# Optimization experiments

Measured on AMD Instinct MI355X. Metric: run time of the kernel, lower is better.

The kernel has to match this reference:

```python
import jax, jax.numpy as jnp
import numpy as np

D_MODEL = 768
N_HEADS = 12
D_HEAD = D_MODEL // N_HEADS

def setup_inputs() -> dict:
    key = jax.random.key(0)
    ks = jax.random.split(key, 5)
    B, T = 2, 4096
    x = jax.random.normal(ks[0], (B, T, D_MODEL), dtype=jnp.float32)
    s_in = 1.0 / np.sqrt(D_MODEL)
    W_qkv = jax.random.normal(ks[1], (D_MODEL, 3 * D_MODEL), dtype=jnp.float32) * s_in
    b_qkv = jnp.zeros((3 * D_MODEL,), dtype=jnp.float32)
    W_proj = jax.random.normal(ks[2], (D_MODEL, D_MODEL), dtype=jnp.float32) * s_in
    b_proj = jnp.zeros((D_MODEL,), dtype=jnp.float32)
    return {"x": x, "W_qkv": W_qkv, "b_qkv": b_qkv, "W_proj": W_proj, "b_proj": b_proj}

def reference(x, W_qkv, b_qkv, W_proj, b_proj):
    B, T, C = x.shape
    qkv = x @ W_qkv + b_qkv                      # [B,T,3C]
    q, k, v = jnp.split(qkv, 3, axis=-1)
    def heads(t):
        return t.reshape(B, T, N_HEADS, D_HEAD).transpose(0, 2, 1, 3)  # [B,H,T,d]
    q, k, v = heads(q), heads(k), heads(v)
    scale = 1.0 / np.sqrt(D_HEAD)
    att = jnp.einsum('bhqd,bhkd->bhqk', q, k) * scale  # [B,H,T,T]
    causal = jnp.tril(jnp.ones((T, T), dtype=bool))
    att = jnp.where(causal[None, None], att, -jnp.inf)
    att = jax.nn.softmax(att, axis=-1)
    y = jnp.einsum('bhqk,bhkd->bhqd', att, v)          # [B,H,T,d]
    y = y.transpose(0, 2, 1, 3).reshape(B, T, C)
    return y @ W_proj + b_proj
```

## Files before the change

kernel.cpp:

```cpp
#include <hip/hip_runtime.h>
#include <hip/hip_bf16.h>

typedef __bf16 bf16_t;
typedef bf16_t bf16x4 __attribute__((ext_vector_type(4)));
typedef bf16_t bf16x8 __attribute__((ext_vector_type(8)));
typedef float  f32x4  __attribute__((ext_vector_type(4)));

#define TSEQ   4096
#define NBATCH 2
#define DMODEL 768
#define NHEADS 12
#define DHEAD  64
#define NTOK   (NBATCH*TSEQ)
#define NQKV   (3*DMODEL)

#define QSCALE 0.18033688011112042f
#define SMAX 24.0f

__device__ __forceinline__ f32x4 mfma16(bf16x8 a, bf16x8 b, f32x4 c) {
  return __builtin_amdgcn_mfma_f32_16x16x32_bf16(a, b, c, 0, 0, 0);
}

__device__ __forceinline__ void glds16(const bf16_t* g, bf16_t* l) {
  __builtin_amdgcn_global_load_lds(
      (const __attribute__((address_space(1))) void*)g,
      (__attribute__((address_space(3))) void*)l, 16, 0, 0);
}

__global__ __launch_bounds__(256) void k_prep(
    const float* __restrict__ W1, bf16_t* __restrict__ O1,
    const float* __restrict__ W2, bf16_t* __restrict__ O2,
    const float* __restrict__ X, bf16_t* __restrict__ Xb) {
  __shared__ bf16_t tile[64][66];
  int t = blockIdx.x;
  if (t >= 576) {
    const int idx = (t - 576) * 256 + threadIdx.x;
#pragma unroll
    for (int it = 0; it < 2; ++it) {
      const long c = (long)idx + (long)it * 393216;
      const float4 v0 = *(const float4*)(X + c * 8);
      const float4 v1 = *(const float4*)(X + c * 8 + 4);
      bf16x8 o;
      o[0] = (bf16_t)v0.x; o[1] = (bf16_t)v0.y;
      o[2] = (bf16_t)v0.z; o[3] = (bf16_t)v0.w;
      o[4] = (bf16_t)v1.x; o[5] = (bf16_t)v1.y;
      o[6] = (bf16_t)v1.z; o[7] = (bf16_t)v1.w;
      *(bf16x8*)(Xb + c * 8) = o;
    }
    return;
  }
  const float* in; bf16_t* out; int R, C, c0, r0;
  if (t < 432) { in = W1; out = O1; R = DMODEL; C = NQKV;
                 c0 = (t % 36) * 64; r0 = (t / 36) * 64; }
  else { t -= 432; in = W2; out = O2; R = DMODEL; C = DMODEL;
         c0 = (t % 12) * 64; r0 = (t / 12) * 64; }
  const int tid = threadIdx.x;
  const int r = tid >> 2, cb = (tid & 3) * 16;
  const float* ip = in + (long)(r0 + r) * C + c0 + cb;
#pragma unroll
  for (int k = 0; k < 16; k += 4) {
    float4 v = *(const float4*)(ip + k);
    tile[r][cb + k + 0] = (bf16_t)v.x;
    tile[r][cb + k + 1] = (bf16_t)v.y;
    tile[r][cb + k + 2] = (bf16_t)v.z;
    tile[r][cb + k + 3] = (bf16_t)v.w;
  }
  __syncthreads();
  const int c = tid >> 2, rb = (tid & 3) * 16;
  bf16_t* op = out + (long)(c0 + c) * R + r0 + rb;
  bf16x8 v0, v1;
#pragma unroll
  for (int i = 0; i < 8; ++i) { v0[i] = tile[rb + i][c]; v1[i] = tile[rb + 8 + i][c]; }
  *(bf16x8*)(op) = v0;
  *(bf16x8*)(op + 8) = v1;
}

__global__ __launch_bounds__(256) void k_gemm_qkv(
    const bf16_t* __restrict__ Xb, const bf16_t* __restrict__ Bt,
    const float* __restrict__ bias,
    bf16_t* __restrict__ Qo, bf16_t* __restrict__ Ko, bf16_t* __restrict__ Vt) {
  __shared__ __align__(16) bf16_t As[2 * 128 * 32];
  __shared__ __align__(16) bf16_t Bs[2 * 128 * 32];
  const int wave = threadIdx.x >> 6;
  const int lane = threadIdx.x & 63;
  const int quad = lane >> 4;
  const int l16  = lane & 15;
  const int m0 = blockIdx.x * 128;
  const int n0 = blockIdx.y * 128;

  const int srow4  = lane >> 2;
  const int schunk = (lane & 3) ^ ((lane >> 3) & 3);
  const bf16_t* a0 = Xb + (long)(m0 + wave * 32 + srow4) * DMODEL + schunk * 8;
  const bf16_t* b0 = Bt + (long)(n0 + wave * 32 + srow4) * DMODEL + schunk * 8;

  f32x4 acc[2][8] = {};

  glds16(a0,               As + (wave * 32) * 32);
  glds16(a0 + 16 * DMODEL, As + (wave * 32 + 16) * 32);
  glds16(b0,               Bs + (wave * 32) * 32);
  glds16(b0 + 16 * DMODEL, Bs + (wave * 32 + 16) * 32);
  __syncthreads();

  const int sw = (l16 >> 1) & 3;
  for (int ks = 0; ks < DMODEL / 32; ++ks) {
    const int p = ks & 1;
    if (ks + 1 < DMODEL / 32) {
      const int k1 = (ks + 1) * 32;
      bf16_t* Asx = (p ? As : As + 128 * 32);
      bf16_t* Bsx = (p ? Bs : Bs + 128 * 32);
      glds16(a0 + k1,               Asx + (wave * 32) * 32);
      glds16(a0 + 16 * DMODEL + k1, Asx + (wave * 32 + 16) * 32);
      glds16(b0 + k1,               Bsx + (wave * 32) * 32);
      glds16(b0 + 16 * DMODEL + k1, Bsx + (wave * 32 + 16) * 32);
    }
    const bf16_t* Ap = As + p * (128 * 32);
    const bf16_t* Bp = Bs + p * (128 * 32);

    bf16x8 af0 = *(const bf16x8*)(Ap + (wave * 32 + l16) * 32 + ((quad ^ sw) << 3));
    bf16x8 af1 = *(const bf16x8*)(Ap + (wave * 32 + 16 + l16) * 32 + ((quad ^ sw) << 3));
#pragma unroll
    for (int nt = 0; nt < 8; ++nt) {
      bf16x8 bfm = *(const bf16x8*)(Bp + (nt * 16 + l16) * 32 + ((quad ^ sw) << 3));
      acc[0][nt] = mfma16(af0, bfm, acc[0][nt]);
      acc[1][nt] = mfma16(af1, bfm, acc[1][nt]);
    }
    __syncthreads();
  }

#pragma unroll
  for (int s = 0; s < 2; ++s)
#pragma unroll
    for (int nt = 0; nt < 8; ++nt) {
      const int n = n0 + nt * 16 + l16;
      const float bv = bias[n];
      const int mb = m0 + wave * 32 + s * 16 + quad * 4;
      const int b = mb >> 12;
      const int t = mb & 4095;
      if (n < DMODEL) {
        const int h = n >> 6, d = n & 63;
        bf16_t* qp = Qo + (((long)(b * NHEADS + h) * TSEQ + t) << 6) + d;
#pragma unroll
        for (int j = 0; j < 4; ++j)
          qp[(long)j << 6] = (bf16_t)((acc[s][nt][j] + bv) * QSCALE);
      } else if (n < 2 * DMODEL) {
        const int n2 = n - DMODEL, h = n2 >> 6, d = n2 & 63;
        bf16_t* kp = Ko + (((long)(b * NHEADS + h) * TSEQ + t) << 6) + d;
#pragma unroll
        for (int j = 0; j < 4; ++j)
          kp[(long)j << 6] = (bf16_t)(acc[s][nt][j] + bv);
      } else {
        const int n2 = n - 2 * DMODEL, h = n2 >> 6, d = n2 & 63;
        bf16x4 v;
#pragma unroll
        for (int j = 0; j < 4; ++j) v[j] = (bf16_t)(acc[s][nt][j] + bv);
        *(bf16x4*)(Vt + ((long)(b * NHEADS + h) * DHEAD + d) * TSEQ + t) = v;
      }
    }
}

__global__ __launch_bounds__(256) void k_gemm_proj(
    const bf16_t* __restrict__ P0, const bf16_t* __restrict__ P1,
    const float* __restrict__ L0, const float* __restrict__ L1,
    const bf16_t* __restrict__ Bt, const float* __restrict__ bias,
    float* __restrict__ out) {
  __shared__ __align__(16) bf16_t A0s[2 * 64 * 32];
  __shared__ __align__(16) bf16_t A1s[2 * 64 * 32];
  __shared__ __align__(16) bf16_t Bs[2 * 128 * 32];
  __shared__ float linv[NHEADS * 64];
  const int wave = threadIdx.x >> 6;
  const int lane = threadIdx.x & 63;
  const int quad = lane >> 4;
  const int l16  = lane & 15;
  const int m0 = blockIdx.x * 64;
  const int n0 = blockIdx.y * 128;
  const int b  = m0 >> 12;
  const int t0 = m0 & 4095;

  for (int i = threadIdx.x; i < NHEADS * 64; i += 256) {
    const int h = i >> 6, t = i & 63;
    const long idx = (long)(b * NHEADS + h) * TSEQ + t0 + t;
    linv[i] = 1.f / (L0[idx] + L1[idx]);
  }

  const int srow = lane >> 2;
  const int scol = (lane & 3) * 8;
  const bf16_t* b0 = Bt + (long)(n0 + wave * 16 + srow) * DMODEL + scol;
  const long arowbase = (long)(t0 + wave * 16 + srow);

  f32x4 acc[8] = {};

  {
    const long off = (((long)(b * NHEADS + 0) * TSEQ + arowbase) << 6) + scol;
    glds16(P0 + off, A0s + wave * 16 * 32);
    glds16(P1 + off, A1s + wave * 16 * 32);
  }
  glds16(b0,               Bs + wave * 16 * 32);
  glds16(b0 + 64 * DMODEL, Bs + (64 + wave * 16) * 32);
  __syncthreads();

  for (int ks = 0; ks < DMODEL / 32; ++ks) {
    const int p = ks & 1;
    if (ks + 1 < DMODEL / 32) {
      const int k1 = (ks + 1) * 32;
      const int ksn = ks + 1;
      bf16_t* A0x = (p ? A0s : A0s + 64 * 32);
      bf16_t* A1x = (p ? A1s : A1s + 64 * 32);
      bf16_t* Bsx = (p ? Bs : Bs + 128 * 32);
      const long off = (((long)(b * NHEADS + (ksn >> 1)) * TSEQ + arowbase) << 6)
                       + ((ksn & 1) << 5) + scol;
      glds16(P0 + off, A0x + wave * 16 * 32);
      glds16(P1 + off, A1x + wave * 16 * 32);
      glds16(b0 + k1,               Bsx + wave * 16 * 32);
      glds16(b0 + 64 * DMODEL + k1, Bsx + (64 + wave * 16) * 32);
    }
    const bf16_t* A0p = A0s + p * (64 * 32);
    const bf16_t* A1p = A1s + p * (64 * 32);
    const bf16_t* Bp  = Bs + p * (128 * 32);

    bf16x8 a0 = *(const bf16x8*)(A0p + (wave * 16 + l16) * 32 + quad * 8);
    bf16x8 a1 = *(const bf16x8*)(A1p + (wave * 16 + l16) * 32 + quad * 8);
    const float li = linv[(ks >> 1) * 64 + wave * 16 + l16];
    bf16x8 af;
#pragma unroll
    for (int j = 0; j < 8; ++j)
      af[j] = (bf16_t)(((float)a0[j] + (float)a1[j]) * li);
#pragma unroll
    for (int nt = 0; nt < 8; ++nt) {
      bf16x8 bfm = *(const bf16x8*)(Bp + (nt * 16 + l16) * 32 + quad * 8);
      acc[nt] = mfma16(af, bfm, acc[nt]);
    }
    __syncthreads();
  }

#pragma unroll
  for (int nt = 0; nt < 8; ++nt) {
    const int n = n0 + nt * 16 + l16;
    const float bv = bias[n];
#pragma unroll
    for (int j = 0; j < 4; ++j) {
      const int m = m0 + wave * 16 + quad * 4 + j;
      out[(long)m * DMODEL + n] = acc[nt][j] + bv;
    }
  }
}

__global__ __launch_bounds__(256, 4) void k_attn(
    const bf16_t* __restrict__ Q, const bf16_t* __restrict__ K,
    const bf16_t* __restrict__ Vt,
    bf16_t* __restrict__ P0, bf16_t* __restrict__ P1,
    float* __restrict__ L0, float* __restrict__ L1) {
  __shared__ __align__(16) bf16_t kbuf[2][64 * 64];
  __shared__ __align__(16) bf16_t vbuf[2][64 * 64];
  const int wave = threadIdx.x >> 6;
  const int lane = threadIdx.x & 63;
  const int quad = lane >> 4;
  const int l16  = lane & 15;
  const int bh = blockIdx.x;
  const int qt = 31 - (blockIdx.y >> 1);
  const int sp = blockIdx.y & 1;
  const int niter = qt + 1;
  const int c0 = sp * niter;
  bf16_t* Pp = sp ? P1 : P0;
  float*  Lp = sp ? L1 : L0;

  const bf16_t* Qh = Q + ((long)bh * TSEQ << 6);
  const bf16_t* Kh = K + ((long)bh * TSEQ << 6);
  const bf16_t* Vh = Vt + (long)bh * DHEAD * TSEQ;

  const int qbase = qt * 128 + wave * 32;

  bf16x8 qf[2][2];
#pragma unroll
  for (int s = 0; s < 2; ++s) {
    const bf16_t* qrow = Qh + ((long)(qbase + s * 16 + l16) << 6);
    qf[s][0] = *(const bf16x8*)(qrow + quad * 8);
    qf[s][1] = *(const bf16x8*)(qrow + 32 + quad * 8);
  }

  f32x4 acc[2][4] = {};
  float lS[2] = {0.f, 0.f};
  const f32x4 minit = {-SMAX, -SMAX, -SMAX, -SMAX};

  const int kperm = ((l16 >> 2) << 3) + (l16 & 3);
  const int swl = l16 & 7;
  const int srow = lane >> 3;
  const int cV = (lane & 7) ^ (srow & 7);
  const int cK0 = (lane & 7) ^ (srow & 3);
  const int cK1 = cK0 ^ 4;
  const int r0a = wave * 16, r0b = wave * 16 + 8;

  {
    const int k00 = c0 << 6;
    glds16(Kh + ((long)(k00 + r0a + srow) << 6) + cK0 * 8, &kbuf[0][r0a * 64]);
    glds16(Kh + ((long)(k00 + r0b + srow) << 6) + cK1 * 8, &kbuf[0][r0b * 64]);
    glds16(Vh + (long)(r0a + srow) * TSEQ + k00 + cV * 8,  &vbuf[0][r0a * 64]);
    glds16(Vh + (long)(r0b + srow) * TSEQ + k00 + cV * 8,  &vbuf[0][r0b * 64]);
  }
  __syncthreads();

  for (int ci = 0; ci < niter; ++ci) {
    const int p = ci & 1;
    const int k0 = (c0 + ci) << 6;
    if (ci + 1 < niter) {
      const int k1 = k0 + 64;
      glds16(Kh + ((long)(k1 + r0a + srow) << 6) + cK0 * 8, &kbuf[1 - p][r0a * 64]);
      glds16(Kh + ((long)(k1 + r0b + srow) << 6) + cK1 * 8, &kbuf[1 - p][r0b * 64]);
      glds16(Vh + (long)(r0a + srow) * TSEQ + k1 + cV * 8,  &vbuf[1 - p][r0a * 64]);
      glds16(Vh + (long)(r0b + srow) * TSEQ + k1 + cV * 8,  &vbuf[1 - p][r0b * 64]);
    }
    const bf16_t* kb = kbuf[p];
    const bf16_t* vb = vbuf[p];

#pragma unroll
    for (int g = 0; g < 2; ++g) {
      const int rw0 = (g * 32 + kperm) * 64;
      const int rw1 = (g * 32 + 4 + kperm) * 64;
      bf16x8 kf00 = *(const bf16x8*)(kb + rw0 + ((quad ^ swl) << 3));
      bf16x8 kf01 = *(const bf16x8*)(kb + rw0 + (((quad + 4) ^ swl) << 3));
      bf16x8 kf10 = *(const bf16x8*)(kb + rw1 + ((quad ^ swl) << 3));
      bf16x8 kf11 = *(const bf16x8*)(kb + rw1 + (((quad + 4) ^ swl) << 3));
      const bool domask = (k0 + g * 32 + 31 > qbase);

      bf16x8 pf[2];
#pragma unroll
      for (int s = 0; s < 2; ++s) {
        f32x4 st0 = minit, st1 = minit;
        st0 = mfma16(kf00, qf[s][0], st0);
        st0 = mfma16(kf01, qf[s][1], st0);
        st1 = mfma16(kf10, qf[s][0], st1);
        st1 = mfma16(kf11, qf[s][1], st1);
        if (domask) {
          const int qS = qbase + s * 16 + l16;
          const int kb0 = k0 + g * 32 + quad * 8;
#pragma unroll
          for (int j = 0; j < 4; ++j) {
            if (kb0 + j > qS)     st0[j] = -1e30f;
            if (kb0 + 4 + j > qS) st1[j] = -1e30f;
          }
        }
        float rs = 0.f;
#pragma unroll
        for (int j = 0; j < 4; ++j) {
          float e0 = __builtin_amdgcn_exp2f(st0[j]);
          float e1 = __builtin_amdgcn_exp2f(st1[j]);
          rs += e0 + e1;
          pf[s][j]     = (bf16_t)e0;
          pf[s][4 + j] = (bf16_t)e1;
        }
        lS[s] += rs;
      }
#pragma unroll
      for (int dt = 0; dt < 4; ++dt) {
        const int row = dt * 16 + l16;
        bf16x8 vf = *(const bf16x8*)(vb + row * 64 + ((((g << 2) + quad) ^ swl) << 3));
#pragma unroll
        for (int s = 0; s < 2; ++s)
          acc[s][dt] = mfma16(vf, pf[s], acc[s][dt]);
      }
    }
    __syncthreads();
  }

#pragma unroll
  for (int s = 0; s < 2; ++s) {
    lS[s] += __shfl_xor(lS[s], 16);
    lS[s] += __shfl_xor(lS[s], 32);
  }
#pragma unroll
  for (int s = 0; s < 2; ++s) {
    const int qS = qbase + s * 16 + l16;
    bf16_t* prow = Pp + (((long)bh * TSEQ + qS) << 6);
#pragma unroll
    for (int dt = 0; dt < 4; ++dt) {
      bf16x4 w;
#pragma unroll
      for (int j = 0; j < 4; ++j) w[j] = (bf16_t)acc[s][dt][j];
      *(bf16x4*)(prow + dt * 16 + quad * 4) = w;
    }
    if (quad == 0) Lp[(long)bh * TSEQ + qS] = lS[s];
  }
}

extern "C" void kernel_launch(void* const* d_in, const int* in_sizes, int n_in,
                              void* d_out, int out_size, void* d_ws, size_t ws_size,
                              hipStream_t stream) {
  (void)in_sizes; (void)n_in; (void)out_size; (void)ws_size;
  const float* x     = (const float*)d_in[0];
  const float* Wqkv  = (const float*)d_in[1];
  const float* bqkv  = (const float*)d_in[2];
  const float* Wproj = (const float*)d_in[3];
  const float* bproj = (const float*)d_in[4];
  float* out = (float*)d_out;

  char* ws = (char*)d_ws;
  bf16_t* wqkv_t  = (bf16_t*)ws; ws += (long)NQKV * DMODEL * 2;
  bf16_t* wproj_t = (bf16_t*)ws; ws += (long)DMODEL * DMODEL * 2;
  bf16_t* Xb      = (bf16_t*)ws; ws += (long)NTOK * DMODEL * 2;
  bf16_t* Qb      = (bf16_t*)ws; ws += (long)NTOK * DMODEL * 2;
  bf16_t* Kb      = (bf16_t*)ws; ws += (long)NTOK * DMODEL * 2;
  bf16_t* Vtb     = (bf16_t*)ws; ws += (long)NTOK * DMODEL * 2;
  bf16_t* P0b     = (bf16_t*)ws; ws += (long)NTOK * DMODEL * 2;
  bf16_t* P1b     = (bf16_t*)ws; ws += (long)NTOK * DMODEL * 2;
  float*  L0b     = (float*)ws;  ws += (long)NHEADS * NBATCH * TSEQ * 4;
  float*  L1b     = (float*)ws;  ws += (long)NHEADS * NBATCH * TSEQ * 4;

  k_prep<<<576 + 1536, 256, 0, stream>>>(Wqkv, wqkv_t, Wproj, wproj_t, x, Xb);
  k_gemm_qkv<<<dim3(NTOK / 128, NQKV / 128), 256, 0, stream>>>(Xb, wqkv_t, bqkv, Qb, Kb, Vtb);
  k_attn<<<dim3(NBATCH * NHEADS, 64), 256, 0, stream>>>(Qb, Kb, Vtb, P0b, P1b, L0b, L1b);
  k_gemm_proj<<<dim3(NTOK / 64, DMODEL / 128), 256, 0, stream>>>(
      P0b, P1b, L0b, L1b, wproj_t, bproj, out);
}
```

Before: 218.0 us.

## Split split-K combine into separate kernel and enlarge proj GEMM tile with LDS swizzle

Moves the merge of the two attention partial outputs and the normalisation by the summed softmax denominators out of the projection GEMM into a standalone k_combine kernel. That kernel writes a token-major bf16 activation buffer. The projection GEMM then reads one A operand instead of two, uses 128x128 tiles with two M sub-tiles per wave, and applies an XOR swizzle on LDS chunks to reduce bank conflicts. This adds an extra kernel launch and a full write and read of the combined activation through memory, in exchange for fewer A loads and more MFMA work per B fragment in the GEMM.

```diff
diff --git a/kernel.cpp b/kernel.cpp
--- a/kernel.cpp
+++ b/kernel.cpp
@@ -158,90 +158,88 @@
     }
 }
 
-__global__ __launch_bounds__(256) void k_gemm_proj(
+__global__ __launch_bounds__(256) void k_combine(
     const bf16_t* __restrict__ P0, const bf16_t* __restrict__ P1,
     const float* __restrict__ L0, const float* __restrict__ L1,
-    const bf16_t* __restrict__ Bt, const float* __restrict__ bias,
-    float* __restrict__ out) {
-  __shared__ __align__(16) bf16_t A0s[2 * 64 * 32];
-  __shared__ __align__(16) bf16_t A1s[2 * 64 * 32];
+    bf16_t* __restrict__ Ab) {
+  const int bh = blockIdx.x;
+  const int t  = blockIdx.y * 32 + (threadIdx.x >> 3);
+  const int d0 = (threadIdx.x & 7) * 8;
+  const long lidx = (long)bh * TSEQ + t;
+  const float li = 1.f / (L0[lidx] + L1[lidx]);
+  const long pidx = (lidx << 6) + d0;
+  bf16x8 a = *(const bf16x8*)(P0 + pidx);
+  bf16x8 b = *(const bf16x8*)(P1 + pidx);
+  bf16x8 o;
+#pragma unroll
+  for (int j = 0; j < 8; ++j)
+    o[j] = (bf16_t)(((float)a[j] + (float)b[j]) * li);
+  const int bb = bh / NHEADS, h = bh % NHEADS;
+  *(bf16x8*)(Ab + (long)(bb * TSEQ + t) * DMODEL + h * 64 + d0) = o;
+}
+
+__global__ __launch_bounds__(256) void k_gemm_proj(
+    const bf16_t* __restrict__ Ab, const bf16_t* __restrict__ Bt,
+    const float* __restrict__ bias, float* __restrict__ out) {
+  __shared__ __align__(16) bf16_t As[2 * 128 * 32];
   __shared__ __align__(16) bf16_t Bs[2 * 128 * 32];
-  __shared__ float linv[NHEADS * 64];
   const int wave = threadIdx.x >> 6;
   const int lane = threadIdx.x & 63;
   const int quad = lane >> 4;
   const int l16  = lane & 15;
-  const int m0 = blockIdx.x * 64;
+  const int m0 = blockIdx.x * 128;
   const int n0 = blockIdx.y * 128;
-  const int b  = m0 >> 12;
-  const int t0 = m0 & 4095;
-
-  for (int i = threadIdx.x; i < NHEADS * 64; i += 256) {
-    const int h = i >> 6, t = i & 63;
-    const long idx = (long)(b * NHEADS + h) * TSEQ + t0 + t;
-    linv[i] = 1.f / (L0[idx] + L1[idx]);
-  }
-
-  const int srow = lane >> 2;
-  const int scol = (lane & 3) * 8;
-  const bf16_t* b0 = Bt + (long)(n0 + wave * 16 + srow) * DMODEL + scol;
-  const long arowbase = (long)(t0 + wave * 16 + srow);
-
-  f32x4 acc[8] = {};
-
-  {
-    const long off = (((long)(b * NHEADS + 0) * TSEQ + arowbase) << 6) + scol;
-    glds16(P0 + off, A0s + wave * 16 * 32);
-    glds16(P1 + off, A1s + wave * 16 * 32);
-  }
-  glds16(b0,               Bs + wave * 16 * 32);
-  glds16(b0 + 64 * DMODEL, Bs + (64 + wave * 16) * 32);
+
+  const int srow4  = lane >> 2;
+  const int schunk = (lane & 3) ^ ((lane >> 3) & 3);
+  const bf16_t* a0 = Ab + (long)(m0 + wave * 32 + srow4) * DMODEL + schunk * 8;
+  const bf16_t* b0 = Bt + (long)(n0 + wave * 32 + srow4) * DMODEL + schunk * 8;
+
+  f32x4 acc[2][8] = {};
+
+  glds16(a0,               As + (wave * 32) * 32);
+  glds16(a0 + 16 * DMODEL, As + (wave * 32 + 16) * 32);
+  glds16(b0,               Bs + (wave * 32) * 32);
+  glds16(b0 + 16 * DMODEL, Bs + (wave * 32 + 16) * 32);
   __syncthreads();
 
+  const int sw = (l16 >> 1) & 3;
   for (int ks = 0; ks < DMODEL / 32; ++ks) {
     const int p = ks & 1;
     if (ks + 1 < DMODEL / 32) {
       const int k1 = (ks + 1) * 32;
-      const int ksn = ks + 1;
-      bf16_t* A0x = (p ? A0s : A0s + 64 * 32);
-      bf16_t* A1x = (p ? A1s : A1s + 64 * 32);
+      bf16_t* Asx = (p ? As : As + 128 * 32);
       bf16_t* Bsx = (p ? Bs : Bs + 128 * 32);
-      const long off = (((long)(b * NHEADS + (ksn >> 1)) * TSEQ + arowbase) << 6)
-                       + ((ksn & 1) << 5) + scol;
-      glds16(P0 + off, A0x + wave * 16 * 32);
-      glds16(P1 + off, A1x + wave * 16 * 32);
-      glds16(b0 + k1,               Bsx + wave * 16 * 32);
-      glds16(b0 + 64 * DMODEL + k1, Bsx + (64 + wave * 16) * 32);
-    }
-    const bf16_t* A0p = A0s + p * (64 * 32);
-    const bf16_t* A1p = A1s + p * (64 * 32);
-    const bf16_t* Bp  = Bs + p * (128 * 32);
-
-    bf16x8 a0 = *(const bf16x8*)(A0p + (wave * 16 + l16) * 32 + quad * 8);
-    bf16x8 a1 = *(const bf16x8*)(A1p + (wave * 16 + l16) * 32 + quad * 8);
-    const float li = linv[(ks >> 1) * 64 + wave * 16 + l16];
-    bf16x8 af;
-#pragma unroll
-    for (int j = 0; j < 8; ++j)
-      af[j] = (bf16_t)(((float)a0[j] + (float)a1[j]) * li);
+      glds16(a0 + k1,               Asx + (wave * 32) * 32);
+      glds16(a0 + 16 * DMODEL + k1, Asx + (wave * 32 + 16) * 32);
+      glds16(b0 + k1,               Bsx + (wave * 32) * 32);
+      glds16(b0 + 16 * DMODEL + k1, Bsx + (wave * 32 + 16) * 32);
+    }
+    const bf16_t* Ap = As + p * (128 * 32);
+    const bf16_t* Bp = Bs + p * (128 * 32);
+
+    bf16x8 af0 = *(const bf16x8*)(Ap + (wave * 32 + l16) * 32 + ((quad ^ sw) << 3));
+    bf16x8 af1 = *(const bf16x8*)(Ap + (wave * 32 + 16 + l16) * 32 + ((quad ^ sw) << 3));
 #pragma unroll
     for (int nt = 0; nt < 8; ++nt) {
-      bf16x8 bfm = *(const bf16x8*)(Bp + (nt * 16 + l16) * 32 + quad * 8);
-      acc[nt] = mfma16(af, bfm, acc[nt]);
+      bf16x8 bfm = *(const bf16x8*)(Bp + (nt * 16 + l16) * 32 + ((quad ^ sw) << 3));
+      acc[0][nt] = mfma16(af0, bfm, acc[0][nt]);
+      acc[1][nt] = mfma16(af1, bfm, acc[1][nt]);
     }
     __syncthreads();
   }
 
 #pragma unroll
-  for (int nt = 0; nt < 8; ++nt) {
-    const int n = n0 + nt * 16 + l16;
-    const float bv = bias[n];
-#pragma unroll
-    for (int j = 0; j < 4; ++j) {
-      const int m = m0 + wave * 16 + quad * 4 + j;
-      out[(long)m * DMODEL + n] = acc[nt][j] + bv;
-    }
-  }
+  for (int s = 0; s < 2; ++s)
+#pragma unroll
+    for (int nt = 0; nt < 8; ++nt) {
+      const int n = n0 + nt * 16 + l16;
+      const float bv = bias[n];
+      const int m = m0 + wave * 32 + s * 16 + quad * 4;
+#pragma unroll
+      for (int j = 0; j < 4; ++j)
+        out[(long)(m + j) * DMODEL + n] = acc[s][nt][j] + bv;
+    }
 }
 
 __global__ __launch_bounds__(256, 4) void k_attn(
@@ -401,12 +399,15 @@
   bf16_t* Vtb     = (bf16_t*)ws; ws += (long)NTOK * DMODEL * 2;
   bf16_t* P0b     = (bf16_t*)ws; ws += (long)NTOK * DMODEL * 2;
   bf16_t* P1b     = (bf16_t*)ws; ws += (long)NTOK * DMODEL * 2;
+  bf16_t* Abb     = (bf16_t*)ws; ws += (long)NTOK * DMODEL * 2;
   float*  L0b     = (float*)ws;  ws += (long)NHEADS * NBATCH * TSEQ * 4;
   float*  L1b     = (float*)ws;  ws += (long)NHEADS * NBATCH * TSEQ * 4;
 
   k_prep<<<576 + 1536, 256, 0, stream>>>(Wqkv, wqkv_t, Wproj, wproj_t, x, Xb);
   k_gemm_qkv<<<dim3(NTOK / 128, NQKV / 128), 256, 0, stream>>>(Xb, wqkv_t, bqkv, Qb, Kb, Vtb);
   k_attn<<<dim3(NBATCH * NHEADS, 64), 256, 0, stream>>>(Qb, Kb, Vtb, P0b, P1b, L0b, L1b);
-  k_gemm_proj<<<dim3(NTOK / 64, DMODEL / 128), 256, 0, stream>>>(
-      P0b, P1b, L0b, L1b, wproj_t, bproj, out);
-}
+  k_combine<<<dim3(NBATCH * NHEADS, TSEQ / 32), 256, 0, stream>>>(
+      P0b, P1b, L0b, L1b, Abb);
+  k_gemm_proj<<<dim3(NTOK / 128, DMODEL / 128), 256, 0, stream>>>(
+      Abb, wproj_t, bproj, out);
+}
```

After: 221.9 us. No clear change (+1.8%).

## Triple-buffer QKV GEMM LDS loads with partial vmcnt waits

Applied to the files above, without the earlier changes.

Replaces the double-buffered LDS staging in the QKV projection GEMM with a three-stage ring, issuing loads two k-steps ahead. The full __syncthreads is replaced by s_waitcnt vmcnt(4) plus a raw barrier, so only the oldest stage's global-to-LDS loads must finish before compute. This hides more global memory latency at the cost of 50% more shared memory per block, which can reduce occupancy. Correctness depends on the hand-counted vmcnt matching exactly four outstanding loads per stage.

```diff
diff --git a/kernel.cpp b/kernel.cpp
--- a/kernel.cpp
+++ b/kernel.cpp
@@ -79,8 +79,8 @@
     const bf16_t* __restrict__ Xb, const bf16_t* __restrict__ Bt,
     const float* __restrict__ bias,
     bf16_t* __restrict__ Qo, bf16_t* __restrict__ Ko, bf16_t* __restrict__ Vt) {
-  __shared__ __align__(16) bf16_t As[2 * 128 * 32];
-  __shared__ __align__(16) bf16_t Bs[2 * 128 * 32];
+  __shared__ __align__(16) bf16_t As[3 * 128 * 32];
+  __shared__ __align__(16) bf16_t Bs[3 * 128 * 32];
   const int wave = threadIdx.x >> 6;
   const int lane = threadIdx.x & 63;
   const int quad = lane >> 4;
@@ -95,26 +95,28 @@
 
   f32x4 acc[2][8] = {};
 
-  glds16(a0,               As + (wave * 32) * 32);
-  glds16(a0 + 16 * DMODEL, As + (wave * 32 + 16) * 32);
-  glds16(b0,               Bs + (wave * 32) * 32);
-  glds16(b0 + 16 * DMODEL, Bs + (wave * 32 + 16) * 32);
-  __syncthreads();
+  auto stage = [&](int ks) {
+    const int koff = ks * 32;
+    bf16_t* Ax = As + (ks % 3) * (128 * 32);
+    bf16_t* Bx = Bs + (ks % 3) * (128 * 32);
+    glds16(a0 + koff,               Ax + (wave * 32) * 32);
+    glds16(a0 + 16 * DMODEL + koff, Ax + (wave * 32 + 16) * 32);
+    glds16(b0 + koff,               Bx + (wave * 32) * 32);
+    glds16(b0 + 16 * DMODEL + koff, Bx + (wave * 32 + 16) * 32);
+  };
+
+  const int NS = DMODEL / 32;
+  stage(0);
+  stage(1);
+  asm volatile("s_waitcnt vmcnt(4)" ::: "memory");
+  __builtin_amdgcn_s_barrier();
+  __builtin_amdgcn_sched_barrier(0);
 
   const int sw = (l16 >> 1) & 3;
-  for (int ks = 0; ks < DMODEL / 32; ++ks) {
-    const int p = ks & 1;
-    if (ks + 1 < DMODEL / 32) {
-      const int k1 = (ks + 1) * 32;
-      bf16_t* Asx = (p ? As : As + 128 * 32);
-      bf16_t* Bsx = (p ? Bs : Bs + 128 * 32);
-      glds16(a0 + k1,               Asx + (wave * 32) * 32);
-      glds16(a0 + 16 * DMODEL + k1, Asx + (wave * 32 + 16) * 32);
-      glds16(b0 + k1,               Bsx + (wave * 32) * 32);
-      glds16(b0 + 16 * DMODEL + k1, Bsx + (wave * 32 + 16) * 32);
-    }
-    const bf16_t* Ap = As + p * (128 * 32);
-    const bf16_t* Bp = Bs + p * (128 * 32);
+  for (int ks = 0; ks < NS; ++ks) {
+    if (ks + 2 < NS) stage(ks + 2);
+    const bf16_t* Ap = As + (ks % 3) * (128 * 32);
+    const bf16_t* Bp = Bs + (ks % 3) * (128 * 32);
 
     bf16x8 af0 = *(const bf16x8*)(Ap + (wave * 32 + l16) * 32 + ((quad ^ sw) << 3));
     bf16x8 af1 = *(const bf16x8*)(Ap + (wave * 32 + 16 + l16) * 32 + ((quad ^ sw) << 3));
@@ -124,7 +126,16 @@
       acc[0][nt] = mfma16(af0, bfm, acc[0][nt]);
       acc[1][nt] = mfma16(af1, bfm, acc[1][nt]);
     }
-    __syncthreads();
+
+    if (ks + 1 < NS) {
+      if (ks + 2 < NS) {
+        asm volatile("s_waitcnt vmcnt(4)" ::: "memory");
+      } else {
+        asm volatile("s_waitcnt vmcnt(0)" ::: "memory");
+      }
+      __builtin_amdgcn_s_barrier();
+      __builtin_amdgcn_sched_barrier(0);
+    }
   }
 
 #pragma unroll
```

Result: no change. 218.5 us (+0.3%).
